# Performance work log

Measured on AMD Instinct MI355X. Metric: run time of the kernel, lower is better.

## Reference

```python
import jax, jax.numpy as jnp
import numpy as np

NUM_JOINTS = 24
IN_DIM = 256      # PoseMLP hidden_dim (per-joint input feature)
HID = 128         # MLP default hidden_dim
OUT_DIM = 6
B = 16384

def setup_inputs() -> dict:
    key = jax.random.key(0)
    ks = jax.random.split(key, 7)
    s1 = 1.0 / np.sqrt(IN_DIM)   # torch Linear init scale (uniform bound)
    s2 = 1.0 / np.sqrt(HID)
    return {
        "pose_feat": jax.random.normal(ks[0], (B, NUM_JOINTS, IN_DIM), dtype=jnp.float32),
        # stacked per-joint weights: Linear stores W as (out, in); we keep (in, out)
        "W1": jax.random.uniform(ks[1], (NUM_JOINTS, IN_DIM, HID), minval=-s1, maxval=s1, dtype=jnp.float32),
        "b1": jax.random.uniform(ks[2], (NUM_JOINTS, HID), minval=-s1, maxval=s1, dtype=jnp.float32),
        "W2": jax.random.uniform(ks[3], (NUM_JOINTS, HID, HID), minval=-s2, maxval=s2, dtype=jnp.float32),
        "b2": jax.random.uniform(ks[4], (NUM_JOINTS, HID), minval=-s2, maxval=s2, dtype=jnp.float32),
        "W3": jax.random.uniform(ks[5], (NUM_JOINTS, HID, OUT_DIM), minval=-s2, maxval=s2, dtype=jnp.float32),
        "b3": jax.random.uniform(ks[6], (NUM_JOINTS, OUT_DIM), minval=-s2, maxval=s2, dtype=jnp.float32),
    }

def reference(pose_feat, W1, b1, W2, b2, W3, b3):
    # Batched per-joint MLPs (fuses the 24 independent small MLPs into 3 grouped GEMMs)
    h = jax.nn.relu(jnp.einsum('bji,jih->bjh', pose_feat, W1) + b1)  # [B,24,128]
    h = jax.nn.relu(jnp.einsum('bjh,jhk->bjk', h, W2) + b2)          # [B,24,128]
    out = jnp.einsum('bjh,jho->bjo', h, W3) + b3                     # [B,24,6]
    return out
```

## Files before the change

kernel.cpp:

```cpp
#include <hip/hip_runtime.h>
#include <hip/hip_fp16.h>

typedef _Float16 half_t;
typedef __attribute__((ext_vector_type(8))) _Float16 half8;
typedef __attribute__((ext_vector_type(4))) _Float16 half4;
typedef __attribute__((ext_vector_type(4))) float floatx4;

#define NJ 24
#define IN_DIM 256
#define HID 128
#define OUT_DIM 6
#define BATCH 16384
#define BM 64

#define W1_JSTRIDE (8 * 128 * 32)
#define W2_JSTRIDE (4 * 128 * 32)
#define W3_JSTRIDE (16 * 128)
#define WT1_ELEMS (NJ * W1_JSTRIDE)
#define WT2_ELEMS (NJ * W2_JSTRIDE)
#define WT3_ELEMS (NJ * W3_JSTRIDE)
#define WT2_OFF WT1_ELEMS
#define WT3_OFF (WT1_ELEMS + WT2_ELEMS)
#define B3P_BYTE_OFF ((size_t)(WT1_ELEMS + WT2_ELEMS + WT3_ELEMS) * 2)
#define PREP_TOTAL (WT1_ELEMS + WT2_ELEMS + WT3_ELEMS + NJ * 16)

__global__ void posemlp_prep(const float* __restrict__ W1, const float* __restrict__ W2,
                             const float* __restrict__ W3, const float* __restrict__ b3,
                             half_t* __restrict__ wt, float* __restrict__ b3p) {
    int t = blockIdx.x * 256 + threadIdx.x;
    if (t < WT1_ELEMS) {
        int j = t / W1_JSTRIDE, r = t % W1_JSTRIDE;
        int ks = r / 4096, r2 = r % 4096;
        int n = r2 / 32, kk = r2 % 32, k = ks * 32 + kk;
        wt[t] = (half_t)W1[((size_t)j * IN_DIM + k) * HID + n];
    } else if (t < WT2_OFF + WT2_ELEMS) {
        int u = t - WT2_OFF;
        int j = u / W2_JSTRIDE, r = u % W2_JSTRIDE;
        int ks = r / 4096, r2 = r % 4096;
        int n = r2 / 32, kk = r2 % 32, k = ks * 32 + kk;
        wt[t] = (half_t)W2[((size_t)j * HID + k) * HID + n];
    } else if (t < WT3_OFF + WT3_ELEMS) {
        int u = t - WT3_OFF;
        int j = u / W3_JSTRIDE, r = u % W3_JSTRIDE;
        int n = r / 128, k = r % 128;
        wt[t] = (n < OUT_DIM) ? (half_t)W3[((size_t)j * HID + k) * OUT_DIM + n] : (half_t)0.0f;
    } else if (t < PREP_TOTAL) {
        int u = t - WT3_OFF - WT3_ELEMS;
        int j = u / 16, n = u % 16;
        b3p[u] = (n < OUT_DIM) ? b3[j * OUT_DIM + n] : 0.0f;
    }
}

__device__ inline void gll16(const void* g, void* l) {
    __builtin_amdgcn_global_load_lds(
        (const __attribute__((address_space(1))) unsigned int*)g,
        (__attribute__((address_space(3))) unsigned int*)l, 16, 0, 0);
}

__device__ inline half8 lds_read8(const half_t* lds, int r, int k) {
    int byte = r * 256 + k * 2;
    byte ^= (r & 7) << 4;
    return *(const half8*)((const char*)lds + byte);
}
__device__ inline void lds_write4(half_t* lds, int r, int n, half4 v) {
    int byte = r * 256 + n * 2;
    byte ^= (r & 7) << 4;
    *(half4*)((char*)lds + byte) = v;
}

__device__ inline half8 cvt8(floatx4 a, floatx4 b) {
    half8 h;
    h[0] = (_Float16)a[0]; h[1] = (_Float16)a[1]; h[2] = (_Float16)a[2]; h[3] = (_Float16)a[3];
    h[4] = (_Float16)b[0]; h[5] = (_Float16)b[1]; h[6] = (_Float16)b[2]; h[7] = (_Float16)b[3];
    return h;
}

__global__ __launch_bounds__(256, 3) void posemlp_main(
    const float* __restrict__ X, const half_t* __restrict__ wt,
    const float* __restrict__ b1, const float* __restrict__ b2,
    const float* __restrict__ b3p, float* __restrict__ out) {
    __shared__ half_t wbuf[16384];
    __shared__ half_t w3buf[2048];
    __shared__ half_t h_lds[BM * HID];

    const int bid0 = blockIdx.x;
    const int bid = (bid0 & 7) * 768 + (bid0 >> 3);
    const int j = bid >> 8;
    const int row0 = (bid & 255) * BM;
    const int tid = threadIdx.x;
    const int w = tid >> 6;
    const int l = tid & 63;
    const int lrow = l & 15;
    const int q = l >> 4;
    const int myrow = w * 16 + lrow;

    const float* xq = X + ((size_t)(row0 + myrow) * NJ + j) * IN_DIM + q * 8;

    const half_t* w1j = wt + (size_t)j * W1_JSTRIDE;
    const half_t* w2j = wt + WT2_OFF + (size_t)j * W2_JSTRIDE;
    const half_t* w3j = wt + WT3_OFF + (size_t)j * W3_JSTRIDE;

    const int sn = tid >> 2, ss = tid & 3;
    const int wsrc = sn * 32 + (ss ^ ((sn >> 1) & 3)) * 8;

    floatx4 px[3][2];
    px[0][0] = *(const floatx4*)(xq);
    px[0][1] = *(const floatx4*)(xq + 4);
    px[1][0] = *(const floatx4*)(xq + 32);
    px[1][1] = *(const floatx4*)(xq + 36);
    px[2][0] = *(const floatx4*)(xq + 64);
    px[2][1] = *(const floatx4*)(xq + 68);
    {
        const int tn = tid >> 4, tsl = tid & 15;
        gll16(w3j + tn * 128 + (tsl ^ tn) * 8, &w3buf[w * 512]);
    }
#pragma unroll
    for (int r = 0; r < 8; ++r)
        gll16(w1j + r * 2048 + wsrc, &wbuf[r * 2048 + w * 512]);
    __syncthreads();

#define L1_ITER(ks, wbbase) do {                                            \
        half8 bx = cvt8(px[(ks) % 3][0], px[(ks) % 3][1]);                  \
        if ((ks) < 5) {                                                     \
            px[(ks) % 3][0] = *(const floatx4*)(xq + ((ks) + 3) * 32);      \
            px[(ks) % 3][1] = *(const floatx4*)(xq + ((ks) + 3) * 32 + 4);  \
        }                                                                   \
        _Pragma("unroll")                                                   \
        for (int nf = 0; nf < 8; ++nf) {                                    \
            const int n = nf * 16 + lrow;                                   \
            half8 a = *(const half8*)&(wbbase)[n * 32 + (q ^ ((n >> 1) & 3)) * 8]; \
            acc[nf] = __builtin_amdgcn_mfma_f32_16x16x32_f16(a, bx, acc[nf], 0, 0, 0); \
        }                                                                   \
    } while (0)

    floatx4 acc[8] = {};
#pragma unroll
    for (int ks = 0; ks < 4; ++ks) L1_ITER(ks, wbuf + ks * 4096);
    __syncthreads();
#pragma unroll
    for (int r = 0; r < 8; ++r)
        gll16(w1j + 16384 + r * 2048 + wsrc, &wbuf[r * 2048 + w * 512]);
    __syncthreads();

#pragma unroll
    for (int ks = 4; ks < 8; ++ks) L1_ITER(ks, wbuf + (ks - 4) * 4096);
    {
        const float* b1j = b1 + j * HID;
#pragma unroll
        for (int nf = 0; nf < 8; ++nf) {
            floatx4 bb = *(const floatx4*)(b1j + nf * 16 + q * 4);
            floatx4 v = acc[nf];
            half4 hv;
#pragma unroll
            for (int i = 0; i < 4; ++i) hv[i] = (_Float16)fmaxf(v[i] + bb[i], 0.0f);
            lds_write4(h_lds, myrow, nf * 16 + q * 4, hv);
        }
    }
    __syncthreads();
#pragma unroll
    for (int r = 0; r < 8; ++r)
        gll16(w2j + r * 2048 + wsrc, &wbuf[r * 2048 + w * 512]);
    __syncthreads();

    floatx4 acc2[8] = {};
#pragma unroll
    for (int ks = 0; ks < 4; ++ks) {
        half8 bh = lds_read8(h_lds, myrow, ks * 32 + q * 8);
#pragma unroll
        for (int nf = 0; nf < 8; ++nf) {
            const int n = nf * 16 + lrow;
            half8 a = *(const half8*)&wbuf[ks * 4096 + n * 32 + (q ^ ((n >> 1) & 3)) * 8];
            acc2[nf] = __builtin_amdgcn_mfma_f32_16x16x32_f16(a, bh, acc2[nf], 0, 0, 0);
        }
    }
    {
        const float* b2j = b2 + j * HID;
#pragma unroll
        for (int nf = 0; nf < 8; ++nf) {
            floatx4 bb = *(const floatx4*)(b2j + nf * 16 + q * 4);
            floatx4 v = acc2[nf];
            half4 hv;
#pragma unroll
            for (int i = 0; i < 4; ++i) hv[i] = (_Float16)fmaxf(v[i] + bb[i], 0.0f);
            lds_write4(h_lds, myrow, nf * 16 + q * 4, hv);
        }
    }

    floatx4 acc3 = {};
#pragma unroll
    for (int ks = 0; ks < 4; ++ks) {
        const int u = ks * 4 + q;
        half8 a3 = *(const half8*)&w3buf[lrow * 128 + (u ^ lrow) * 8];
        half8 bh = lds_read8(h_lds, myrow, ks * 32 + q * 8);
        acc3 = __builtin_amdgcn_mfma_f32_16x16x32_f16(a3, bh, acc3, 0, 0, 0);
    }
    {
        floatx4 bb = *(const floatx4*)(b3p + j * 16 + q * 4);
        const int orow = row0 + myrow;
        float* op = out + ((size_t)orow * NJ + j) * OUT_DIM;
        floatx4 v = acc3;
        if (q == 0) {
            float2 s0 = {v[0] + bb[0], v[1] + bb[1]};
            float2 s1 = {v[2] + bb[2], v[3] + bb[3]};
            *(float2*)(op + 0) = s0;
            *(float2*)(op + 2) = s1;
        } else if (q == 1) {
            float2 s = {v[0] + bb[0], v[1] + bb[1]};
            *(float2*)(op + 4) = s;
        }
    }
}

extern "C" void kernel_launch(void* const* d_in, const int* in_sizes, int n_in,
                              void* d_out, int out_size, void* d_ws, size_t ws_size,
                              hipStream_t stream) {
    const float* X  = (const float*)d_in[0];
    const float* W1 = (const float*)d_in[1];
    const float* b1 = (const float*)d_in[2];
    const float* W2 = (const float*)d_in[3];
    const float* b2 = (const float*)d_in[4];
    const float* W3 = (const float*)d_in[5];
    const float* b3 = (const float*)d_in[6];
    float* out = (float*)d_out;

    half_t* wt = (half_t*)d_ws;
    float* b3p = (float*)((char*)d_ws + B3P_BYTE_OFF);

    int prep_blocks = (PREP_TOTAL + 255) / 256;
    posemlp_prep<<<prep_blocks, 256, 0, stream>>>(W1, W2, W3, b3, wt, b3p);

    int grid = NJ * (BATCH / BM);
    posemlp_main<<<grid, 256, 0, stream>>>(X, wt, b1, b2, b3p, out);
}
```

Measured before the change: 132.1 us.

## Prefetch all X chunks up front and use manual waitcnt barriers

Issues all eight X feature loads for layer 1 at kernel start, after the W1/W3 LDS loads, instead of a rolling three-deep register prefetch. Replaces __syncthreads with explicit vmcnt/lgkmcnt waits and pinned s_barrier. The first barrier only waits for the weight loads (vmcnt 16), so the X loads can stay in flight. This aims to keep more global loads outstanding and avoid over-conservative waits, at the cost of extra registers (16 floatx4), which may reduce occupancy under launch_bounds 3.

```diff
diff --git a/kernel.cpp b/kernel.cpp
--- a/kernel.cpp
+++ b/kernel.cpp
@@ -57,6 +57,23 @@
         (__attribute__((address_space(3))) unsigned int*)l, 16, 0, 0);
 }
 
+#define VMWAIT(N) asm volatile("s_waitcnt vmcnt(" #N ")" ::: "memory")
+#define LGKM0()                                            \
+    do {                                                   \
+        asm volatile("s_waitcnt lgkmcnt(0)" ::: "memory"); \
+        __builtin_amdgcn_sched_barrier(0);                 \
+    } while (0)
+#define FENCE()                                 \
+    do {                                        \
+        asm volatile("" ::: "memory");          \
+        __builtin_amdgcn_sched_barrier(0);      \
+    } while (0)
+__device__ inline void barrier_pinned() {
+    __builtin_amdgcn_sched_barrier(0);
+    __builtin_amdgcn_s_barrier();
+    __builtin_amdgcn_sched_barrier(0);
+}
+
 __device__ inline half8 lds_read8(const half_t* lds, int r, int k) {
     int byte = r * 256 + k * 2;
     byte ^= (r & 7) << 4;
@@ -103,47 +120,54 @@
     const int sn = tid >> 2, ss = tid & 3;
     const int wsrc = sn * 32 + (ss ^ ((sn >> 1) & 3)) * 8;
 
-    floatx4 px[3][2];
-    px[0][0] = *(const floatx4*)(xq);
-    px[0][1] = *(const floatx4*)(xq + 4);
-    px[1][0] = *(const floatx4*)(xq + 32);
-    px[1][1] = *(const floatx4*)(xq + 36);
-    px[2][0] = *(const floatx4*)(xq + 64);
-    px[2][1] = *(const floatx4*)(xq + 68);
+#pragma unroll
+    for (int r = 0; r < 8; ++r)
+        gll16(w1j + r * 2048 + wsrc, &wbuf[r * 2048 + w * 512]);
     {
         const int tn = tid >> 4, tsl = tid & 15;
         gll16(w3j + tn * 128 + (tsl ^ tn) * 8, &w3buf[w * 512]);
     }
-#pragma unroll
-    for (int r = 0; r < 8; ++r)
-        gll16(w1j + r * 2048 + wsrc, &wbuf[r * 2048 + w * 512]);
-    __syncthreads();
-
-#define L1_ITER(ks, wbbase) do {                                            \
-        half8 bx = cvt8(px[(ks) % 3][0], px[(ks) % 3][1]);                  \
-        if ((ks) < 5) {                                                     \
-            px[(ks) % 3][0] = *(const floatx4*)(xq + ((ks) + 3) * 32);      \
-            px[(ks) % 3][1] = *(const floatx4*)(xq + ((ks) + 3) * 32 + 4);  \
-        }                                                                   \
-        _Pragma("unroll")                                                   \
-        for (int nf = 0; nf < 8; ++nf) {                                    \
-            const int n = nf * 16 + lrow;                                   \
-            half8 a = *(const half8*)&(wbbase)[n * 32 + (q ^ ((n >> 1) & 3)) * 8]; \
-            acc[nf] = __builtin_amdgcn_mfma_f32_16x16x32_f16(a, bx, acc[nf], 0, 0, 0); \
-        }                                                                   \
-    } while (0)
+    FENCE();
+    floatx4 px[8][2];
+#pragma unroll
+    for (int c = 0; c < 8; ++c) {
+        px[c][0] = *(const floatx4*)(xq + c * 32);
+        px[c][1] = *(const floatx4*)(xq + c * 32 + 4);
+    }
+    FENCE();
+    VMWAIT(16);
+    barrier_pinned();
 
     floatx4 acc[8] = {};
 #pragma unroll
-    for (int ks = 0; ks < 4; ++ks) L1_ITER(ks, wbuf + ks * 4096);
-    __syncthreads();
+    for (int ks = 0; ks < 4; ++ks) {
+        half8 bx = cvt8(px[ks][0], px[ks][1]);
+#pragma unroll
+        for (int nf = 0; nf < 8; ++nf) {
+            const int n = nf * 16 + lrow;
+            half8 a = *(const half8*)&wbuf[ks * 4096 + n * 32 + (q ^ ((n >> 1) & 3)) * 8];
+            acc[nf] = __builtin_amdgcn_mfma_f32_16x16x32_f16(a, bx, acc[nf], 0, 0, 0);
+        }
+    }
+    LGKM0();
+    barrier_pinned();
 #pragma unroll
     for (int r = 0; r < 8; ++r)
         gll16(w1j + 16384 + r * 2048 + wsrc, &wbuf[r * 2048 + w * 512]);
-    __syncthreads();
-
-#pragma unroll
-    for (int ks = 4; ks < 8; ++ks) L1_ITER(ks, wbuf + (ks - 4) * 4096);
+    FENCE();
+    VMWAIT(0);
+    barrier_pinned();
+
+#pragma unroll
+    for (int ks = 4; ks < 8; ++ks) {
+        half8 bx = cvt8(px[ks][0], px[ks][1]);
+#pragma unroll
+        for (int nf = 0; nf < 8; ++nf) {
+            const int n = nf * 16 + lrow;
+            half8 a = *(const half8*)&wbuf[(ks - 4) * 4096 + n * 32 + (q ^ ((n >> 1) & 3)) * 8];
+            acc[nf] = __builtin_amdgcn_mfma_f32_16x16x32_f16(a, bx, acc[nf], 0, 0, 0);
+        }
+    }
     {
         const float* b1j = b1 + j * HID;
 #pragma unroll
@@ -156,11 +180,14 @@
             lds_write4(h_lds, myrow, nf * 16 + q * 4, hv);
         }
     }
-    __syncthreads();
+    LGKM0();
+    barrier_pinned();
 #pragma unroll
     for (int r = 0; r < 8; ++r)
         gll16(w2j + r * 2048 + wsrc, &wbuf[r * 2048 + w * 512]);
-    __syncthreads();
+    FENCE();
+    VMWAIT(0);
+    barrier_pinned();
 
     floatx4 acc2[8] = {};
 #pragma unroll
```

Result: faster. 119.6 us (-9.5%).

## Read weights directly from global memory and double rows per block

Applied to the files above, without the earlier changes.

Drops the LDS staging of the W1, W2 and W3 tiles and the block-wide barriers around it; each lane now loads its weight fragments straight from the prepacked global buffer, relying on L2. Block size grows from 64 to 128 rows: each wave handles two 16-row fragments, so every weight fragment feeds two MFMAs, and the X prefetch is deepened. The hidden activations stay in per-wave rows of LDS, so only compiler ordering barriers are used and no __syncthreads remains. The trade-off is many more global/L2 weight loads per wave, more registers, and occupancy lowered to 2 blocks per SIMD in the launch bounds.

```diff
diff --git a/kernel.cpp b/kernel.cpp
--- a/kernel.cpp
+++ b/kernel.cpp
@@ -11,7 +11,7 @@
 #define HID 128
 #define OUT_DIM 6
 #define BATCH 16384
-#define BM 64
+#define BM 128
 
 #define W1_JSTRIDE (8 * 128 * 32)
 #define W2_JSTRIDE (4 * 128 * 32)
@@ -51,11 +51,7 @@
     }
 }
 
-__device__ inline void gll16(const void* g, void* l) {
-    __builtin_amdgcn_global_load_lds(
-        (const __attribute__((address_space(1))) unsigned int*)g,
-        (__attribute__((address_space(3))) unsigned int*)l, 16, 0, 0);
-}
+#define ORDER() asm volatile("" ::: "memory")
 
 __device__ inline half8 lds_read8(const half_t* lds, int r, int k) {
     int byte = r * 256 + k * 2;
@@ -75,138 +71,129 @@
     return h;
 }
 
-__global__ __launch_bounds__(256, 3) void posemlp_main(
+__global__ __launch_bounds__(256, 2) void posemlp_main(
     const float* __restrict__ X, const half_t* __restrict__ wt,
     const float* __restrict__ b1, const float* __restrict__ b2,
     const float* __restrict__ b3p, float* __restrict__ out) {
-    __shared__ half_t wbuf[16384];
-    __shared__ half_t w3buf[2048];
     __shared__ half_t h_lds[BM * HID];
 
     const int bid0 = blockIdx.x;
-    const int bid = (bid0 & 7) * 768 + (bid0 >> 3);
-    const int j = bid >> 8;
-    const int row0 = (bid & 255) * BM;
+    const int bid = (bid0 & 7) * 384 + (bid0 >> 3);
+    const int j = bid >> 7;
+    const int row0 = (bid & 127) * BM;
     const int tid = threadIdx.x;
     const int w = tid >> 6;
     const int l = tid & 63;
     const int lrow = l & 15;
     const int q = l >> 4;
-    const int myrow = w * 16 + lrow;
-
-    const float* xq = X + ((size_t)(row0 + myrow) * NJ + j) * IN_DIM + q * 8;
+
+    const int rb = w * 32 + lrow;
+    const float* xr0 = X + ((size_t)(row0 + rb) * NJ + j) * IN_DIM + q * 8;
+    const float* xr1 = X + ((size_t)(row0 + rb + 16) * NJ + j) * IN_DIM + q * 8;
 
     const half_t* w1j = wt + (size_t)j * W1_JSTRIDE;
     const half_t* w2j = wt + WT2_OFF + (size_t)j * W2_JSTRIDE;
     const half_t* w3j = wt + WT3_OFF + (size_t)j * W3_JSTRIDE;
 
-    const int sn = tid >> 2, ss = tid & 3;
-    const int wsrc = sn * 32 + (ss ^ ((sn >> 1) & 3)) * 8;
-
-    floatx4 px[3][2];
-    px[0][0] = *(const floatx4*)(xq);
-    px[0][1] = *(const floatx4*)(xq + 4);
-    px[1][0] = *(const floatx4*)(xq + 32);
-    px[1][1] = *(const floatx4*)(xq + 36);
-    px[2][0] = *(const floatx4*)(xq + 64);
-    px[2][1] = *(const floatx4*)(xq + 68);
-    {
-        const int tn = tid >> 4, tsl = tid & 15;
-        gll16(w3j + tn * 128 + (tsl ^ tn) * 8, &w3buf[w * 512]);
-    }
-#pragma unroll
-    for (int r = 0; r < 8; ++r)
-        gll16(w1j + r * 2048 + wsrc, &wbuf[r * 2048 + w * 512]);
-    __syncthreads();
-
-#define L1_ITER(ks, wbbase) do {                                            \
-        half8 bx = cvt8(px[(ks) % 3][0], px[(ks) % 3][1]);                  \
-        if ((ks) < 5) {                                                     \
-            px[(ks) % 3][0] = *(const floatx4*)(xq + ((ks) + 3) * 32);      \
-            px[(ks) % 3][1] = *(const floatx4*)(xq + ((ks) + 3) * 32 + 4);  \
-        }                                                                   \
-        _Pragma("unroll")                                                   \
-        for (int nf = 0; nf < 8; ++nf) {                                    \
-            const int n = nf * 16 + lrow;                                   \
-            half8 a = *(const half8*)&(wbbase)[n * 32 + (q ^ ((n >> 1) & 3)) * 8]; \
-            acc[nf] = __builtin_amdgcn_mfma_f32_16x16x32_f16(a, bx, acc[nf], 0, 0, 0); \
-        }                                                                   \
-    } while (0)
-
-    floatx4 acc[8] = {};
-#pragma unroll
-    for (int ks = 0; ks < 4; ++ks) L1_ITER(ks, wbuf + ks * 4096);
-    __syncthreads();
-#pragma unroll
-    for (int r = 0; r < 8; ++r)
-        gll16(w1j + 16384 + r * 2048 + wsrc, &wbuf[r * 2048 + w * 512]);
-    __syncthreads();
-
-#pragma unroll
-    for (int ks = 4; ks < 8; ++ks) L1_ITER(ks, wbuf + (ks - 4) * 4096);
+    floatx4 px[4][2][2];
+#pragma unroll
+    for (int c = 0; c < 4; ++c) {
+        px[c][0][0] = *(const floatx4*)(xr0 + c * 32);
+        px[c][0][1] = *(const floatx4*)(xr0 + c * 32 + 4);
+        px[c][1][0] = *(const floatx4*)(xr1 + c * 32);
+        px[c][1][1] = *(const floatx4*)(xr1 + c * 32 + 4);
+    }
+
+    floatx4 acc[8][2] = {};
+#pragma unroll
+    for (int ks = 0; ks < 8; ++ks) {
+        half8 bx0 = cvt8(px[ks & 3][0][0], px[ks & 3][0][1]);
+        half8 bx1 = cvt8(px[ks & 3][1][0], px[ks & 3][1][1]);
+        if (ks < 4) {
+            px[ks & 3][0][0] = *(const floatx4*)(xr0 + (ks + 4) * 32);
+            px[ks & 3][0][1] = *(const floatx4*)(xr0 + (ks + 4) * 32 + 4);
+            px[ks & 3][1][0] = *(const floatx4*)(xr1 + (ks + 4) * 32);
+            px[ks & 3][1][1] = *(const floatx4*)(xr1 + (ks + 4) * 32 + 4);
+        }
+#pragma unroll
+        for (int nf = 0; nf < 8; ++nf) {
+            half8 a = *(const half8*)&w1j[ks * 4096 + (nf * 16 + lrow) * 32 + q * 8];
+            acc[nf][0] = __builtin_amdgcn_mfma_f32_16x16x32_f16(a, bx0, acc[nf][0], 0, 0, 0);
+            acc[nf][1] = __builtin_amdgcn_mfma_f32_16x16x32_f16(a, bx1, acc[nf][1], 0, 0, 0);
+        }
+    }
     {
         const float* b1j = b1 + j * HID;
 #pragma unroll
         for (int nf = 0; nf < 8; ++nf) {
             floatx4 bb = *(const floatx4*)(b1j + nf * 16 + q * 4);
-            floatx4 v = acc[nf];
-            half4 hv;
-#pragma unroll
-            for (int i = 0; i < 4; ++i) hv[i] = (_Float16)fmaxf(v[i] + bb[i], 0.0f);
-            lds_write4(h_lds, myrow, nf * 16 + q * 4, hv);
-        }
-    }
-    __syncthreads();
-#pragma unroll
-    for (int r = 0; r < 8; ++r)
-        gll16(w2j + r * 2048 + wsrc, &wbuf[r * 2048 + w * 512]);
-    __syncthreads();
-
-    floatx4 acc2[8] = {};
+#pragma unroll
+            for (int mf = 0; mf < 2; ++mf) {
+                floatx4 v = acc[nf][mf];
+                half4 hv;
+#pragma unroll
+                for (int i = 0; i < 4; ++i) hv[i] = (_Float16)fmaxf(v[i] + bb[i], 0.0f);
+                lds_write4(h_lds, w * 32 + mf * 16 + lrow, nf * 16 + q * 4, hv);
+            }
+        }
+    }
+    ORDER();
+
+    floatx4 acc2[8][2] = {};
 #pragma unroll
     for (int ks = 0; ks < 4; ++ks) {
-        half8 bh = lds_read8(h_lds, myrow, ks * 32 + q * 8);
-#pragma unroll
-        for (int nf = 0; nf < 8; ++nf) {
-            const int n = nf * 16 + lrow;
-            half8 a = *(const half8*)&wbuf[ks * 4096 + n * 32 + (q ^ ((n >> 1) & 3)) * 8];
-            acc2[nf] = __builtin_amdgcn_mfma_f32_16x16x32_f16(a, bh, acc2[nf], 0, 0, 0);
-        }
-    }
+        half8 bh0 = lds_read8(h_lds, w * 32 + lrow, ks * 32 + q * 8);
+        half8 bh1 = lds_read8(h_lds, w * 32 + 16 + lrow, ks * 32 + q * 8);
+#pragma unroll
+        for (int nf = 0; nf < 8; ++nf) {
+            half8 a = *(const half8*)&w2j[ks * 4096 + (nf * 16 + lrow) * 32 + q * 8];
+            acc2[nf][0] = __builtin_amdgcn_mfma_f32_16x16x32_f16(a, bh0, acc2[nf][0], 0, 0, 0);
+            acc2[nf][1] = __builtin_amdgcn_mfma_f32_16x16x32_f16(a, bh1, acc2[nf][1], 0, 0, 0);
+        }
+    }
+    ORDER();
     {
         const float* b2j = b2 + j * HID;
 #pragma unroll
         for (int nf = 0; nf < 8; ++nf) {
             floatx4 bb = *(const floatx4*)(b2j + nf * 16 + q * 4);
-            floatx4 v = acc2[nf];
-            half4 hv;
-#pragma unroll
-            for (int i = 0; i < 4; ++i) hv[i] = (_Float16)fmaxf(v[i] + bb[i], 0.0f);
-            lds_write4(h_lds, myrow, nf * 16 + q * 4, hv);
-        }
-    }
-
-    floatx4 acc3 = {};
+#pragma unroll
+            for (int mf = 0; mf < 2; ++mf) {
+                floatx4 v = acc2[nf][mf];
+                half4 hv;
+#pragma unroll
+                for (int i = 0; i < 4; ++i) hv[i] = (_Float16)fmaxf(v[i] + bb[i], 0.0f);
+                lds_write4(h_lds, w * 32 + mf * 16 + lrow, nf * 16 + q * 4, hv);
+            }
+        }
+    }
+    ORDER();
+
+    floatx4 acc3[2] = {};
 #pragma unroll
     for (int ks = 0; ks < 4; ++ks) {
-        const int u = ks * 4 + q;
-        half8 a3 = *(const half8*)&w3buf[lrow * 128 + (u ^ lrow) * 8];
-        half8 bh = lds_read8(h_lds, myrow, ks * 32 + q * 8);
-        acc3 = __builtin_amdgcn_mfma_f32_16x16x32_f16(a3, bh, acc3, 0, 0, 0);
+        half8 a3 = *(const half8*)&w3j[lrow * 128 + (ks * 4 + q) * 8];
+        half8 bh0 = lds_read8(h_lds, w * 32 + lrow, ks * 32 + q * 8);
+        half8 bh1 = lds_read8(h_lds, w * 32 + 16 + lrow, ks * 32 + q * 8);
+        acc3[0] = __builtin_amdgcn_mfma_f32_16x16x32_f16(a3, bh0, acc3[0], 0, 0, 0);
+        acc3[1] = __builtin_amdgcn_mfma_f32_16x16x32_f16(a3, bh1, acc3[1], 0, 0, 0);
     }
     {
         floatx4 bb = *(const floatx4*)(b3p + j * 16 + q * 4);
-        const int orow = row0 + myrow;
-        float* op = out + ((size_t)orow * NJ + j) * OUT_DIM;
-        floatx4 v = acc3;
-        if (q == 0) {
-            float2 s0 = {v[0] + bb[0], v[1] + bb[1]};
-            float2 s1 = {v[2] + bb[2], v[3] + bb[3]};
-            *(float2*)(op + 0) = s0;
-            *(float2*)(op + 2) = s1;
-        } else if (q == 1) {
-            float2 s = {v[0] + bb[0], v[1] + bb[1]};
-            *(float2*)(op + 4) = s;
+#pragma unroll
+        for (int mf = 0; mf < 2; ++mf) {
+            const int orow = row0 + w * 32 + mf * 16 + lrow;
+            float* op = out + ((size_t)orow * NJ + j) * OUT_DIM;
+            floatx4 v = acc3[mf];
+            if (q == 0) {
+                float2 s0 = {v[0] + bb[0], v[1] + bb[1]};
+                float2 s1 = {v[2] + bb[2], v[3] + bb[3]};
+                *(float2*)(op + 0) = s0;
+                *(float2*)(op + 2) = s1;
+            } else if (q == 1) {
+                float2 s = {v[0] + bb[0], v[1] + bb[1]};
+                *(float2*)(op + 4) = s;
+            }
         }
     }
 }
```

Measured after the change: 182.5 us. +38.2%, slower.
